# Kernel tuning notes

Measured on AMD Instinct MI355X. Metric: run time of the kernel, lower is better.

The kernel has to match this reference:

```python
import jax, jax.numpy as jnp
import numpy as np

EPS = 1e-5

def _bn(x, g, b):
    # BatchNorm1d, training-mode forward (biased batch stats)
    m = x.mean(axis=0)
    v = x.var(axis=0)
    return (x - m) * jax.lax.rsqrt(v + EPS) * g + b

def setup_inputs() -> dict:
    key = jax.random.key(0)
    ks = jax.random.split(key, 24)
    B, P, Cin, Cout, share, shrink, r = 8, 4096, 64, 128, 8, 4, 8
    k = 2 * r
    mid = Cout // shrink
    s = 0.05
    inp = {
        'points': jax.random.normal(ks[0], (B, P, 2), jnp.float32),
        'features': jax.random.normal(ks[1], (B * P, Cin), jnp.float32),
        # modules_1: Linear(2+Cin -> k), Bilinear(k,k -> k)
        'W1': jax.random.normal(ks[2], (k, 2 + Cin)) * s,
        'b1': jax.random.normal(ks[3], (k,)) * s,
        'Wb': jax.random.normal(ks[4], (k, k, k)) * s,
        'bb': jax.random.normal(ks[5], (k,)) * s,
        # linear_p: Linear(2->2, no bias), BN(2), ReLU, Linear(2->Cout)
        'Wp1': jax.random.normal(ks[6], (2, 2)) * s,
        'gp': jnp.ones((2,)), 'bp': jnp.zeros((2,)),
        'Wp2': jax.random.normal(ks[7], (Cout, 2)) * s,
        'bp2': jax.random.normal(ks[8], (Cout,)) * s,
        # modules_2: Linear(2k->mid,nb)+BN, Linear(mid->mid/share,nb)+BN, Linear(->Cout/share)
        'W2a': jax.random.normal(ks[9], (mid, 2 * k)) * s,
        'g2a': jnp.ones((mid,)), 'b2a': jnp.zeros((mid,)),
        'W2b': jax.random.normal(ks[10], (mid // share, mid)) * s,
        'g2b': jnp.ones((mid // share,)), 'b2b': jnp.zeros((mid // share,)),
        'W2c': jax.random.normal(ks[11], (Cout // share, mid // share)) * s,
        'b2c': jax.random.normal(ks[12], (Cout // share,)) * s,
        # modules_3: Linear(Cin -> Cout)
        'W3': jax.random.normal(ks[13], (Cout, Cin)) * s,
        'b3': jax.random.normal(ks[14], (Cout,)) * s,
        'radius': r,
        'share_planes': share,
    }
    return inp

def reference(points, features, W1, b1, Wb, bb, Wp1, gp, bp, Wp2, bp2,
              W2a, g2a, b2a, W2b, g2b, b2b, W2c, b2c, W3, b3,
              radius, share_planes):
    B, P, _ = points.shape
    k = 2 * radius
    # circular grouping index: neighbors (i+o) mod P, o in [-r..-1, 1..r]
    offsets = jnp.concatenate([jnp.arange(-radius, 0), jnp.arange(1, radius + 1)])
    nn = (jnp.arange(P)[:, None] + offsets[None, :]) % P            # [P, k]
    idx = (jnp.arange(B)[:, None, None] * P + nn[None]).reshape(-1) # [B*P*k]

    pts = points.reshape(-1, 2)                                     # [N, 2]
    nn_pts = pts[idx].reshape(-1, k, 2)                             # [N, k, 2]
    trans = (nn_pts - pts[:, None, :]).reshape(-1, 2)               # [N*k, 2]
    nn_feat = features[idx]                                         # [N*k, Cin]

    # modules_1: Linear -> ReLU -> Bilinear(e, e)
    e = jax.nn.relu(jnp.concatenate([trans, nn_feat], axis=1) @ W1.T + b1)
    energy = jnp.einsum('ni,oij,nj->no', e, Wb, e) + bb             # [N*k, k]

    # linear_p
    p = jax.nn.relu(_bn(trans @ Wp1.T, gp, bp))
    p_embed = p @ Wp2.T + bp2                                       # [N*k, Cout]
    Cout = p_embed.shape[1]

    # shrink_p: split Cout into (a, k), sum over a
    pe = p_embed.reshape(-1, k, Cout // k, k)
    shrink = pe.sum(axis=2).reshape(-1, k)                          # [N*k, k]

    # modules_2: MLP + softmax over neighbor axis
    w = jnp.concatenate([energy, shrink], axis=1)
    w = jax.nn.relu(_bn(w @ W2a.T, g2a, b2a))
    w = jax.nn.relu(_bn(w @ W2b.T, g2b, b2b))
    w = w @ W2c.T + b2c                                             # [N*k, Cout/share]
    w = jax.nn.softmax(w.reshape(-1, k, Cout // share_planes), axis=1)

    # modules_3 + gather + combine
    v = (features @ W3.T + b3)[idx].reshape(-1, k, Cout)
    a = v + p_embed.reshape(-1, k, Cout)
    a = a.reshape(-1, k, share_planes, Cout // share_planes)
    outputs = (a * w[:, :, None, :]).reshape(-1, k, Cout)           # [N, k, Cout]
    return outputs, trans, idx

if __name__ == '__main__':
    out = reference(**setup_inputs())
    print(out[0].shape, out[1].shape, out[2].shape)
```

## Files before the change

### kernel.cpp

```cpp
#include <hip/hip_runtime.h>

#define DEV static __device__ __forceinline__

namespace {
constexpr int PB   = 4096;
constexpr int NPTS = 32768;
constexpr int RR   = 8;
constexpr int K    = 16;
constexpr int COUT = 128;
constexpr int NK   = NPTS * K;
constexpr float BN_EPS = 1e-5f;

constexpr int    WS_SUM1 = 0;
constexpr int    WS_SUM2 = 4;
constexpr int    WS_SUM3 = 68;
constexpr size_t WS_P2   = 256;
constexpr size_t WS_W1   = WS_P2 + 2048 * 64;
constexpr size_t WS_W2   = WS_W1 + (size_t)NK * 16;
}

typedef __attribute__((ext_vector_type(8))) __bf16 bf16x8;
typedef __attribute__((ext_vector_type(4))) float  f32x4;

DEV int nbr_idx(int n, int j) {
    int b = n >> 12, i = n & (PB - 1);
    int o = (j < RR) ? (j - RR) : (j - RR + 1);
    return (b << 12) | ((i + o + PB) & (PB - 1));
}
DEV float wave_sum(float v) {
    #pragma unroll
    for (int off = 32; off >= 1; off >>= 1) v += __shfl_xor(v, off);
    return v;
}
DEV bf16x8 cvt8(float4 a, float4 b) {
    bf16x8 r;
    r[0] = (__bf16)a.x; r[1] = (__bf16)a.y; r[2] = (__bf16)a.z; r[3] = (__bf16)a.w;
    r[4] = (__bf16)b.x; r[5] = (__bf16)b.y; r[6] = (__bf16)b.z; r[7] = (__bf16)b.w;
    return r;
}
DEV float bflo(unsigned u) { union { unsigned x; float f; } c; c.x = u << 16; return c.f; }
DEV float bfhi(unsigned u) { union { unsigned x; float f; } c; c.x = u & 0xffff0000u; return c.f; }
DEV void wave_fence() {
    asm volatile("s_waitcnt lgkmcnt(0)" ::: "memory");
    __builtin_amdgcn_sched_barrier(0);
}

__global__ __launch_bounds__(256) void k_pre(const float* __restrict__ pts,
                                             const float* __restrict__ Wp1,
                                             float* __restrict__ ws)
{
    __shared__ float red[4][4];
    const int t = threadIdx.x, w = t >> 6;
    const float wp10 = Wp1[0], wp11 = Wp1[1], wp12 = Wp1[2], wp13 = Wp1[3];
    float a[4] = {0.f, 0.f, 0.f, 0.f};
    #pragma unroll
    for (int it = 0; it < 4; ++it) {
        const int row = blockIdx.x * 1024 + it * 256 + t;
        const int n = row >> 4, j = row & 15;
        const int idxr = nbr_idx(n, j);
        const float2 pn = ((const float2*)pts)[n];
        const float2 pq = ((const float2*)pts)[idxr];
        const float tx = pq.x - pn.x, ty = pq.y - pn.y;
        const float p10 = wp10 * tx + wp11 * ty;
        const float p11 = wp12 * tx + wp13 * ty;
        a[0] += p10; a[1] += p11; a[2] += p10 * p10; a[3] += p11 * p11;
    }
    #pragma unroll
    for (int q = 0; q < 4; ++q) {
        float s = wave_sum(a[q]);
        if ((t & 63) == 0) red[w][q] = s;
    }
    __syncthreads();
    if (t < 4) atomicAdd(&ws[WS_SUM1 + t], red[0][t] + red[1][t] + red[2][t] + red[3][t]);
}

__global__ __launch_bounds__(256) void k_stage1(
    const float* __restrict__ pts, const float* __restrict__ feat,
    const float* __restrict__ W1, const float* __restrict__ b1,
    const float* __restrict__ Wb, const float* __restrict__ bb,
    const float* __restrict__ Wp1, const float* __restrict__ Wp2,
    const float* __restrict__ bp2, const float* __restrict__ gp,
    const float* __restrict__ bp, const float* __restrict__ W2a,
    float* __restrict__ out_trans, float* __restrict__ out_idx,
    float* __restrict__ ws)
{
    __shared__ float es[4][16][36];
    __shared__ float sA0[16], sA1[16], sA2[16];
    __shared__ float red[4][64];

    const int t = threadIdx.x, w = t >> 6, l = t & 63, c0 = l & 15, jg = l >> 4;
    const int bid = blockIdx.x;
    const int n0 = ((bid & 7) * 256 + (bid >> 3)) * 16 + w * 4;

    if (t < 16) {
        float a0 = 0.f, a1 = 0.f, a2 = 0.f;
        for (int a8 = 0; a8 < 8; ++a8) {
            const int cc = a8 * 16 + t;
            a0 += Wp2[2 * cc]; a1 += Wp2[2 * cc + 1]; a2 += bp2[cc];
        }
        sA0[t] = a0; sA1[t] = a1; sA2[t] = a2;
    }

    const float invM = 1.f / (float)NK;
    const float m0 = ws[WS_SUM1 + 0] * invM, m1 = ws[WS_SUM1 + 1] * invM;
    const float q0 = ws[WS_SUM1 + 2] * invM, q1 = ws[WS_SUM1 + 3] * invM;
    const float sc1x = gp[0] * rsqrtf(q0 - m0 * m0 + BN_EPS);
    const float sc1y = gp[1] * rsqrtf(q1 - m1 * m1 + BN_EPS);
    const float sh1x = fmaf(-m0, sc1x, bp[0]), sh1y = fmaf(-m1, sc1y, bp[1]);
    const float wp10 = Wp1[0], wp11 = Wp1[1], wp12 = Wp1[2], wp13 = Wp1[3];

    const float w1cx = W1[c0 * 66], w1cy = W1[c0 * 66 + 1];
    const float b1c = b1[c0], bbc = bb[c0];
    bf16x8 w1b[2];
    #pragma unroll
    for (int kf = 0; kf < 2; ++kf) {
        const float* p = W1 + c0 * 66 + 2 + kf * 32 + jg * 8;
        const float2 v0 = *(const float2*)(p),     v1 = *(const float2*)(p + 2);
        const float2 v2 = *(const float2*)(p + 4), v3 = *(const float2*)(p + 6);
        w1b[kf] = cvt8(make_float4(v0.x, v0.y, v1.x, v1.y),
                       make_float4(v2.x, v2.y, v3.x, v3.y));
    }
    bf16x8 wbb[8];
    #pragma unroll
    for (int g = 0; g < 8; ++g) {
        const float4* p = (const float4*)(Wb + c0 * 256 + g * 32 + jg * 8);
        wbb[g] = cvt8(p[0], p[1]);
    }
    bf16x8 w2ab[2];
    #pragma unroll
    for (int tq = 0; tq < 2; ++tq) {
        const float4* p = (const float4*)(W2a + (c0 + 16 * tq) * 32 + jg * 8);
        w2ab[tq] = cvt8(p[0], p[1]);
    }

    int idxr[4]; float txv[4], tyv[4], ph0v[4], ph1v[4];
    bf16x8 fa0[4], fa1[4];
    #pragma unroll
    for (int nn = 0; nn < 4; ++nn) {
        const int n = n0 + nn;
        idxr[nn] = nbr_idx(n, c0);
        const float2 pn = ((const float2*)pts)[n];
        const float2 pq = ((const float2*)pts)[idxr[nn]];
        txv[nn] = pq.x - pn.x; tyv[nn] = pq.y - pn.y;
        const float p10 = wp10 * txv[nn] + wp11 * tyv[nn];
        const float p11 = wp12 * txv[nn] + wp13 * tyv[nn];
        ph0v[nn] = fmaxf(fmaf(p10, sc1x, sh1x), 0.f);
        ph1v[nn] = fmaxf(fmaf(p11, sc1y, sh1y), 0.f);
        const float4* fb = (const float4*)(feat + (size_t)idxr[nn] * 64 + jg * 8);
        fa0[nn] = cvt8(fb[0], fb[1]);
        fa1[nn] = cvt8(fb[8], fb[9]);
        if (jg == 0) {
            ((float2*)out_trans)[n * 16 + c0] = make_float2(txv[nn], tyv[nn]);
            out_idx[n * 16 + c0] = (float)idxr[nn];
        }
    }

    float s10 = 0.f, s11 = 0.f, s20 = 0.f, s21 = 0.f;
    __syncthreads();

    #pragma unroll
    for (int nn = 0; nn < 4; ++nn) {
        f32x4 acc;
        #pragma unroll
        for (int r = 0; r < 4; ++r) {
            const int row = jg * 4 + r;
            const float trx = __shfl(txv[nn], row);
            const float tryv = __shfl(tyv[nn], row);
            acc[r] = b1c + w1cx * trx + w1cy * tryv;
        }
        acc = __builtin_amdgcn_mfma_f32_16x16x32_bf16(fa0[nn], w1b[0], acc, 0, 0, 0);
        acc = __builtin_amdgcn_mfma_f32_16x16x32_bf16(fa1[nn], w1b[1], acc, 0, 0, 0);
        #pragma unroll
        for (int r = 0; r < 4; ++r) es[w][jg * 4 + r][c0] = fmaxf(acc[r], 0.f);
        wave_fence();

        const float4 ef0 = *(const float4*)&es[w][c0][0];
        const float4 ef1 = *(const float4*)&es[w][c0][4];
        const float4 ef2 = *(const float4*)&es[w][c0][8];
        const float4 ef3 = *(const float4*)&es[w][c0][12];
        const float ev[16] = {ef0.x, ef0.y, ef0.z, ef0.w, ef1.x, ef1.y, ef1.z, ef1.w,
                              ef2.x, ef2.y, ef2.z, ef2.w, ef3.x, ef3.y, ef3.z, ef3.w};
        const bool hi = (jg & 1);
        const bool ih = (jg >> 1);
        float eh[8];
        #pragma unroll
        for (int e = 0; e < 8; ++e) eh[e] = hi ? ev[8 + e] : ev[e];
        f32x4 acc2;
        #pragma unroll
        for (int r = 0; r < 4; ++r) acc2[r] = bbc;
        #pragma unroll
        for (int g = 0; g < 8; ++g) {
            const float ei = ih ? ev[2 * g + 1] : ev[2 * g];
            bf16x8 a2;
            #pragma unroll
            for (int e = 0; e < 8; ++e) a2[e] = (__bf16)(ei * eh[e]);
            acc2 = __builtin_amdgcn_mfma_f32_16x16x32_bf16(a2, wbb[g], acc2, 0, 0, 0);
        }
        #pragma unroll
        for (int r = 0; r < 4; ++r) es[w][jg * 4 + r][16 + c0] = acc2[r];
        wave_fence();

        bf16x8 xa;
        if (jg < 2) {
            const float* src = &es[w][c0][16 + jg * 8];
            #pragma unroll
            for (int e = 0; e < 8; ++e) xa[e] = (__bf16)src[e];
        } else {
            const int off = (jg - 2) * 8;
            #pragma unroll
            for (int e = 0; e < 8; ++e)
                xa[e] = (__bf16)fmaf(ph0v[nn], sA0[off + e],
                                     fmaf(ph1v[nn], sA1[off + e], sA2[off + e]));
        }
        const f32x4 z4 = {0.f, 0.f, 0.f, 0.f};
        f32x4 w1a0 = __builtin_amdgcn_mfma_f32_16x16x32_bf16(xa, w2ab[0], z4, 0, 0, 0);
        f32x4 w1a1 = __builtin_amdgcn_mfma_f32_16x16x32_bf16(xa, w2ab[1], z4, 0, 0, 0);
        #pragma unroll
        for (int r = 0; r < 4; ++r) {
            s10 += w1a0[r]; s20 += w1a0[r] * w1a0[r];
            s11 += w1a1[r]; s21 += w1a1[r] * w1a1[r];
        }
        wave_fence();

        #pragma unroll
        for (int r = 0; r < 4; ++r) {
            es[w][jg * 4 + r][c0]      = w1a0[r];
            es[w][jg * 4 + r][16 + c0] = w1a1[r];
        }
        wave_fence();

        {
            const int row = l >> 2, ch = l & 3;
            const float* src = &es[w][row][ch * 8];
            bf16x8 pk;
            #pragma unroll
            for (int e = 0; e < 8; ++e) pk[e] = (__bf16)src[e];
            reinterpret_cast<bf16x8*>(ws + WS_W1)[(size_t)((n0 + nn) * 16 + row) * 4 + ch] = pk;
        }
        wave_fence();
    }

    #pragma unroll
    for (int off = 16; off <= 32; off <<= 1) {
        s10 += __shfl_xor(s10, off); s11 += __shfl_xor(s11, off);
        s20 += __shfl_xor(s20, off); s21 += __shfl_xor(s21, off);
    }
    if (jg == 0) {
        red[w][c0] = s10; red[w][16 + c0] = s11;
        red[w][32 + c0] = s20; red[w][48 + c0] = s21;
    }
    __syncthreads();
    if (t < 64)
        (ws + WS_P2)[(size_t)bid * 64 + t] = red[0][t] + red[1][t] + red[2][t] + red[3][t];
}

__global__ __launch_bounds__(256) void k_red2(float* __restrict__ ws)
{
    __shared__ float red[4][64];
    const int t = threadIdx.x, c = t & 63, g = t >> 6;
    const float* P = ws + WS_P2;
    float s = 0.f;
    for (int r = blockIdx.x * 256 + g; r < (blockIdx.x + 1) * 256; r += 4)
        s += P[(size_t)r * 64 + c];
    red[g][c] = s;
    __syncthreads();
    if (t < 64) atomicAdd(&ws[WS_SUM2 + t], red[0][t] + red[1][t] + red[2][t] + red[3][t]);
}

__global__ __launch_bounds__(256) void k_stage3(
    const float* __restrict__ g2a, const float* __restrict__ b2a,
    const float* __restrict__ W2b, float* __restrict__ ws)
{
    __shared__ float sc2s[32], sh2s[32], w2bs[128];
    __shared__ float red[4][8];
    const int t = threadIdx.x, w = t >> 6, l = t & 63;
    if (t < 32) {
        const float invM = 1.f / (float)NK;
        const float m = ws[WS_SUM2 + t] * invM, q = ws[WS_SUM2 + 32 + t] * invM;
        const float sc = g2a[t] * rsqrtf(q - m * m + BN_EPS);
        sc2s[t] = sc; sh2s[t] = fmaf(-m, sc, b2a[t]);
    }
    if (t < 128) w2bs[t] = W2b[t];
    __syncthreads();

    const size_t row = (size_t)blockIdx.x * 256 + t;
    const uint4* w1u = reinterpret_cast<const uint4*>(ws + WS_W1) + row * 4;
    float h[32];
    #pragma unroll
    for (int i = 0; i < 4; ++i) {
        const uint4 u = w1u[i];
        h[i*8+0] = bflo(u.x); h[i*8+1] = bfhi(u.x);
        h[i*8+2] = bflo(u.y); h[i*8+3] = bfhi(u.y);
        h[i*8+4] = bflo(u.z); h[i*8+5] = bfhi(u.z);
        h[i*8+6] = bflo(u.w); h[i*8+7] = bfhi(u.w);
    }
    float acc[4] = {0.f, 0.f, 0.f, 0.f};
    #pragma unroll
    for (int q = 0; q < 32; ++q) {
        const float hv = fmaxf(fmaf(h[q], sc2s[q], sh2s[q]), 0.f);
        #pragma unroll
        for (int p = 0; p < 4; ++p) acc[p] = fmaf(w2bs[p * 32 + q], hv, acc[p]);
    }
    ((float4*)(ws + WS_W2))[row] = make_float4(acc[0], acc[1], acc[2], acc[3]);

    float r8[8] = {acc[0], acc[1], acc[2], acc[3],
                   acc[0]*acc[0], acc[1]*acc[1], acc[2]*acc[2], acc[3]*acc[3]};
    #pragma unroll
    for (int i = 0; i < 8; ++i) r8[i] = wave_sum(r8[i]);
    if (l == 0) {
        #pragma unroll
        for (int i = 0; i < 8; ++i) red[w][i] = r8[i];
    }
    __syncthreads();
    if (t < 8) atomicAdd(&ws[WS_SUM3 + t], red[0][t] + red[1][t] + red[2][t] + red[3][t]);
}

__global__ __launch_bounds__(256) void k_stage4(
    const float* __restrict__ feat, const float* __restrict__ Wp1,
    const float* __restrict__ Wp2, const float* __restrict__ bp2,
    const float* __restrict__ W2c, const float* __restrict__ b2c,
    const float* __restrict__ W3, const float* __restrict__ b3,
    const float* __restrict__ gp, const float* __restrict__ bp,
    const float* __restrict__ g2b, const float* __restrict__ b2b,
    const float* __restrict__ out_trans, const float* __restrict__ ws,
    float* __restrict__ out)
{
    __shared__ bf16x8 w3lds[1024];
    __shared__ float4 pA[32], pB[32], pC[32];
    __shared__ float4 w2c4[16];
    __shared__ float  b2cs[16];

    const int t = threadIdx.x, w = t >> 6, l = t & 63, c0 = l & 15, jg = l >> 4;
    const int bid = blockIdx.x;
    const int n0 = ((bid & 7) * 256 + (bid >> 3)) * 16 + w * 4;

    for (int f = t; f < 1024; f += 256) {
        const int s = f >> 7, kf = (f >> 6) & 1, l2 = f & 63;
        const float4* p = (const float4*)(W3 + (size_t)(16 * s + (l2 & 15)) * 64
                                          + kf * 32 + (l2 >> 4) * 8);
        w3lds[f] = cvt8(p[0], p[1]);
    }
    if (t < 32) {
        const int s = t >> 2, cc = 16 * s + (t & 3) * 4;
        pA[t] = make_float4(Wp2[2*cc], Wp2[2*cc+2], Wp2[2*cc+4], Wp2[2*cc+6]);
        pB[t] = make_float4(Wp2[2*cc+1], Wp2[2*cc+3], Wp2[2*cc+5], Wp2[2*cc+7]);
        pC[t] = make_float4(bp2[cc] + b3[cc], bp2[cc+1] + b3[cc+1],
                            bp2[cc+2] + b3[cc+2], bp2[cc+3] + b3[cc+3]);
    }
    if (t < 16) {
        w2c4[t] = make_float4(W2c[4*t], W2c[4*t+1], W2c[4*t+2], W2c[4*t+3]);
        b2cs[t] = b2c[t];
    }

    const float invM = 1.f / (float)NK;
    const float m0 = ws[WS_SUM1 + 0] * invM, m1 = ws[WS_SUM1 + 1] * invM;
    const float q0 = ws[WS_SUM1 + 2] * invM, q1 = ws[WS_SUM1 + 3] * invM;
    const float sc1x = gp[0] * rsqrtf(q0 - m0 * m0 + BN_EPS);
    const float sc1y = gp[1] * rsqrtf(q1 - m1 * m1 + BN_EPS);
    const float sh1x = fmaf(-m0, sc1x, bp[0]), sh1y = fmaf(-m1, sc1y, bp[1]);
    const float wp10 = Wp1[0], wp11 = Wp1[1], wp12 = Wp1[2], wp13 = Wp1[3];
    float sc3[4], sh3[4];
    #pragma unroll
    for (int p = 0; p < 4; ++p) {
        const float m = ws[WS_SUM3 + p] * invM, q = ws[WS_SUM3 + 4 + p] * invM;
        sc3[p] = g2b[p] * rsqrtf(q - m * m + BN_EPS);
        sh3[p] = fmaf(-m, sc3[p], b2b[p]);
    }

    int idxr[4]; float2 trv[4]; float4 qv[4];
    bf16x8 fa0[4], fa1[4];
    #pragma unroll
    for (int nn = 0; nn < 4; ++nn) {
        const int n = n0 + nn;
        idxr[nn] = nbr_idx(n, c0);
        const float4* fb = (const float4*)(feat + (size_t)idxr[nn] * 64 + jg * 8);
        fa0[nn] = cvt8(fb[0], fb[1]);
        fa1[nn] = cvt8(fb[8], fb[9]);
        trv[nn] = ((const float2*)out_trans)[n * 16 + c0];
        qv[nn]  = ((const float4*)(ws + WS_W2))[n * 16 + c0];
    }
    __syncthreads();

    #pragma unroll
    for (int nn = 0; nn < 4; ++nn) {
        const int n = n0 + nn;
        const float p10 = wp10 * trv[nn].x + wp11 * trv[nn].y;
        const float p11 = wp12 * trv[nn].x + wp13 * trv[nn].y;
        const float ph0 = fmaxf(fmaf(p10, sc1x, sh1x), 0.f);
        const float ph1 = fmaxf(fmaf(p11, sc1y, sh1y), 0.f);
        const float h0 = fmaxf(fmaf(qv[nn].x, sc3[0], sh3[0]), 0.f);
        const float h1 = fmaxf(fmaf(qv[nn].y, sc3[1], sh3[1]), 0.f);
        const float h2 = fmaxf(fmaf(qv[nn].z, sc3[2], sh3[2]), 0.f);
        const float h3 = fmaxf(fmaf(qv[nn].w, sc3[3], sh3[3]), 0.f);
        float wsm[4];
        #pragma unroll
        for (int r = 0; r < 4; ++r) {
            const int c = jg * 4 + r;
            const float4 wc = w2c4[c];
            const float lgv = b2cs[c] + wc.x * h0 + wc.y * h1 + wc.z * h2 + wc.w * h3;
            float mx = lgv;
            #pragma unroll
            for (int off = 1; off <= 8; off <<= 1) mx = fmaxf(mx, __shfl_xor(mx, off));
            const float ex = __expf(lgv - mx);
            float ss = ex;
            #pragma unroll
            for (int off = 1; off <= 8; off <<= 1) ss += __shfl_xor(ss, off);
            wsm[r] = ex / ss;
        }
        float* ob = out + (size_t)(n * 16 + c0) * COUT;
        #pragma unroll
        for (int s = 0; s < 8; ++s) {
            const float4 a4 = pA[s * 4 + jg], b4 = pB[s * 4 + jg], c4 = pC[s * 4 + jg];
            f32x4 ci;
            ci[0] = fmaf(ph0, a4.x, fmaf(ph1, b4.x, c4.x));
            ci[1] = fmaf(ph0, a4.y, fmaf(ph1, b4.y, c4.y));
            ci[2] = fmaf(ph0, a4.z, fmaf(ph1, b4.z, c4.z));
            ci[3] = fmaf(ph0, a4.w, fmaf(ph1, b4.w, c4.w));
            ci = __builtin_amdgcn_mfma_f32_16x16x32_bf16(w3lds[s * 128 + l],      fa0[nn], ci, 0, 0, 0);
            ci = __builtin_amdgcn_mfma_f32_16x16x32_bf16(w3lds[s * 128 + 64 + l], fa1[nn], ci, 0, 0, 0);
            *(float4*)(ob + 16 * s + jg * 4) =
                make_float4(ci[0] * wsm[0], ci[1] * wsm[1], ci[2] * wsm[2], ci[3] * wsm[3]);
        }
    }
}

extern "C" void kernel_launch(void* const* d_in, const int* in_sizes, int n_in,
                              void* d_out, int out_size, void* d_ws, size_t ws_size,
                              hipStream_t stream)
{
    const float* pts  = (const float*)d_in[0];
    const float* feat = (const float*)d_in[1];
    const float* W1   = (const float*)d_in[2];
    const float* b1   = (const float*)d_in[3];
    const float* Wb   = (const float*)d_in[4];
    const float* bb   = (const float*)d_in[5];
    const float* Wp1  = (const float*)d_in[6];
    const float* gp   = (const float*)d_in[7];
    const float* bp   = (const float*)d_in[8];
    const float* Wp2  = (const float*)d_in[9];
    const float* bp2  = (const float*)d_in[10];
    const float* W2a  = (const float*)d_in[11];
    const float* g2a  = (const float*)d_in[12];
    const float* b2a  = (const float*)d_in[13];
    const float* W2b  = (const float*)d_in[14];
    const float* g2b  = (const float*)d_in[15];
    const float* b2b  = (const float*)d_in[16];
    const float* W2c  = (const float*)d_in[17];
    const float* b2c  = (const float*)d_in[18];
    const float* W3   = (const float*)d_in[19];
    const float* b3   = (const float*)d_in[20];

    float* out       = (float*)d_out;
    float* out_trans = out + (size_t)NK * COUT;
    float* out_idx   = out_trans + (size_t)NK * 2;
    float* ws        = (float*)d_ws;

    hipMemsetAsync(ws, 0, 256 * sizeof(float), stream);
    k_pre<<<512, 256, 0, stream>>>(pts, Wp1, ws);
    k_stage1<<<2048, 256, 0, stream>>>(pts, feat, W1, b1, Wb, bb, Wp1, Wp2, bp2,
                                       gp, bp, W2a, out_trans, out_idx, ws);
    k_red2<<<8, 256, 0, stream>>>(ws);
    k_stage3<<<2048, 256, 0, stream>>>(g2a, b2a, W2b, ws);
    k_stage4<<<2048, 256, 0, stream>>>(feat, Wp1, Wp2, bp2, W2c, b2c, W3, b3,
                                       gp, bp, g2b, b2b, out_trans, ws, out);
}
```

Measured before the change: 260.2 us.

## Fuse all stages into one persistent kernel with software grid barriers

Replaces the five separate launches (pre-stats, stage1, partial reduction, stage3, stage4) with one persistent kernel of 512 blocks. The blocks synchronise through atomic-counter grid barriers in the workspace, and BN statistics are accumulated with direct atomics instead of a separate reduction kernel. The final stage double-buffers neighbour loads, and the softmax max-subtraction is dropped. This removes launch gaps and tail effects. The cost is reliance on all 512 blocks being co-resident, and on the barrier counter being reset by the memset, otherwise the barriers could deadlock. Removing the max-subtraction also risks exp overflow.

```diff
diff --git a/kernel.cpp b/kernel.cpp
--- a/kernel.cpp
+++ b/kernel.cpp
@@ -9,13 +9,15 @@
 constexpr int K    = 16;
 constexpr int COUT = 128;
 constexpr int NK   = NPTS * K;
+constexpr int GRID = 512;
+constexpr int NPB  = NPTS / GRID;
 constexpr float BN_EPS = 1e-5f;
 
 constexpr int    WS_SUM1 = 0;
 constexpr int    WS_SUM2 = 4;
 constexpr int    WS_SUM3 = 68;
-constexpr size_t WS_P2   = 256;
-constexpr size_t WS_W1   = WS_P2 + 2048 * 64;
+constexpr int    WS_BAR  = 96;
+constexpr size_t WS_W1   = 256;
 constexpr size_t WS_W2   = WS_W1 + (size_t)NK * 16;
 }
 
@@ -45,52 +47,54 @@
     __builtin_amdgcn_sched_barrier(0);
 }
 
-__global__ __launch_bounds__(256) void k_pre(const float* __restrict__ pts,
-                                             const float* __restrict__ Wp1,
-                                             float* __restrict__ ws)
-{
-    __shared__ float red[4][4];
-    const int t = threadIdx.x, w = t >> 6;
-    const float wp10 = Wp1[0], wp11 = Wp1[1], wp12 = Wp1[2], wp13 = Wp1[3];
-    float a[4] = {0.f, 0.f, 0.f, 0.f};
-    #pragma unroll
-    for (int it = 0; it < 4; ++it) {
-        const int row = blockIdx.x * 1024 + it * 256 + t;
-        const int n = row >> 4, j = row & 15;
-        const int idxr = nbr_idx(n, j);
-        const float2 pn = ((const float2*)pts)[n];
-        const float2 pq = ((const float2*)pts)[idxr];
-        const float tx = pq.x - pn.x, ty = pq.y - pn.y;
-        const float p10 = wp10 * tx + wp11 * ty;
-        const float p11 = wp12 * tx + wp13 * ty;
-        a[0] += p10; a[1] += p11; a[2] += p10 * p10; a[3] += p11 * p11;
-    }
-    #pragma unroll
-    for (int q = 0; q < 4; ++q) {
-        float s = wave_sum(a[q]);
-        if ((t & 63) == 0) red[w][q] = s;
-    }
+DEV void grid_barrier(int* cnt) {
     __syncthreads();
-    if (t < 4) atomicAdd(&ws[WS_SUM1 + t], red[0][t] + red[1][t] + red[2][t] + red[3][t]);
-}
-
-__global__ __launch_bounds__(256) void k_stage1(
+    if (threadIdx.x == 0) {
+        __threadfence();
+        __hip_atomic_fetch_add(cnt, 1, __ATOMIC_ACQ_REL, __HIP_MEMORY_SCOPE_AGENT);
+        int spins = 0;
+        while (__hip_atomic_load(cnt, __ATOMIC_ACQUIRE, __HIP_MEMORY_SCOPE_AGENT) < GRID
+               && spins < (1 << 24)) {
+            __builtin_amdgcn_s_sleep(2);
+            ++spins;
+        }
+        __threadfence();
+    }
+    __syncthreads();
+}
+
+__global__ __launch_bounds__(256, 2) void k_mega(
     const float* __restrict__ pts, const float* __restrict__ feat,
     const float* __restrict__ W1, const float* __restrict__ b1,
     const float* __restrict__ Wb, const float* __restrict__ bb,
-    const float* __restrict__ Wp1, const float* __restrict__ Wp2,
-    const float* __restrict__ bp2, const float* __restrict__ gp,
-    const float* __restrict__ bp, const float* __restrict__ W2a,
-    float* __restrict__ out_trans, float* __restrict__ out_idx,
-    float* __restrict__ ws)
+    const float* __restrict__ Wp1, const float* __restrict__ gp,
+    const float* __restrict__ bp, const float* __restrict__ Wp2,
+    const float* __restrict__ bp2, const float* __restrict__ W2a,
+    const float* __restrict__ g2a, const float* __restrict__ b2a,
+    const float* __restrict__ W2b, const float* __restrict__ g2b,
+    const float* __restrict__ b2b, const float* __restrict__ W2c,
+    const float* __restrict__ b2c, const float* __restrict__ W3,
+    const float* __restrict__ b3,
+    float* __restrict__ out, float* __restrict__ out_trans,
+    float* __restrict__ out_idx, float* __restrict__ ws)
 {
-    __shared__ float es[4][16][36];
-    __shared__ float sA0[16], sA1[16], sA2[16];
-    __shared__ float red[4][64];
+    __shared__ float  es[4][16][36];
+    __shared__ float  sA0[16], sA1[16], sA2[16];
+    __shared__ float  redl[4][64];
+    __shared__ bf16x8 w3lds[1024];
+    __shared__ float4 pA[32], pB[32], pC[32];
+    __shared__ float4 w2c4[16];
+    __shared__ float  b2cs[16];
+    __shared__ float  sc2s[32], sh2s[32], w2bs[128];
 
     const int t = threadIdx.x, w = t >> 6, l = t & 63, c0 = l & 15, jg = l >> 4;
     const int bid = blockIdx.x;
-    const int n0 = ((bid & 7) * 256 + (bid >> 3)) * 16 + w * 4;
+    const int swz = (bid & 7) * (GRID / 8) + (bid >> 3);
+    const int n_base = swz * NPB;
+    int* bar = (int*)(ws + WS_BAR);
+
+    const float wp10 = Wp1[0], wp11 = Wp1[1], wp12 = Wp1[2], wp13 = Wp1[3];
+    const float invM = 1.f / (float)NK;
 
     if (t < 16) {
         float a0 = 0.f, a1 = 0.f, a2 = 0.f;
@@ -101,326 +105,314 @@
         sA0[t] = a0; sA1[t] = a1; sA2[t] = a2;
     }
 
-    const float invM = 1.f / (float)NK;
-    const float m0 = ws[WS_SUM1 + 0] * invM, m1 = ws[WS_SUM1 + 1] * invM;
-    const float q0 = ws[WS_SUM1 + 2] * invM, q1 = ws[WS_SUM1 + 3] * invM;
-    const float sc1x = gp[0] * rsqrtf(q0 - m0 * m0 + BN_EPS);
-    const float sc1y = gp[1] * rsqrtf(q1 - m1 * m1 + BN_EPS);
-    const float sh1x = fmaf(-m0, sc1x, bp[0]), sh1y = fmaf(-m1, sc1y, bp[1]);
-    const float wp10 = Wp1[0], wp11 = Wp1[1], wp12 = Wp1[2], wp13 = Wp1[3];
-
-    const float w1cx = W1[c0 * 66], w1cy = W1[c0 * 66 + 1];
-    const float b1c = b1[c0], bbc = bb[c0];
-    bf16x8 w1b[2];
-    #pragma unroll
-    for (int kf = 0; kf < 2; ++kf) {
-        const float* p = W1 + c0 * 66 + 2 + kf * 32 + jg * 8;
-        const float2 v0 = *(const float2*)(p),     v1 = *(const float2*)(p + 2);
-        const float2 v2 = *(const float2*)(p + 4), v3 = *(const float2*)(p + 6);
-        w1b[kf] = cvt8(make_float4(v0.x, v0.y, v1.x, v1.y),
-                       make_float4(v2.x, v2.y, v3.x, v3.y));
-    }
-    bf16x8 wbb[8];
-    #pragma unroll
-    for (int g = 0; g < 8; ++g) {
-        const float4* p = (const float4*)(Wb + c0 * 256 + g * 32 + jg * 8);
-        wbb[g] = cvt8(p[0], p[1]);
-    }
-    bf16x8 w2ab[2];
-    #pragma unroll
-    for (int tq = 0; tq < 2; ++tq) {
-        const float4* p = (const float4*)(W2a + (c0 + 16 * tq) * 32 + jg * 8);
-        w2ab[tq] = cvt8(p[0], p[1]);
-    }
-
-    int idxr[4]; float txv[4], tyv[4], ph0v[4], ph1v[4];
-    bf16x8 fa0[4], fa1[4];
-    #pragma unroll
-    for (int nn = 0; nn < 4; ++nn) {
-        const int n = n0 + nn;
-        idxr[nn] = nbr_idx(n, c0);
-        const float2 pn = ((const float2*)pts)[n];
-        const float2 pq = ((const float2*)pts)[idxr[nn]];
-        txv[nn] = pq.x - pn.x; tyv[nn] = pq.y - pn.y;
-        const float p10 = wp10 * txv[nn] + wp11 * tyv[nn];
-        const float p11 = wp12 * txv[nn] + wp13 * tyv[nn];
-        ph0v[nn] = fmaxf(fmaf(p10, sc1x, sh1x), 0.f);
-        ph1v[nn] = fmaxf(fmaf(p11, sc1y, sh1y), 0.f);
-        const float4* fb = (const float4*)(feat + (size_t)idxr[nn] * 64 + jg * 8);
-        fa0[nn] = cvt8(fb[0], fb[1]);
-        fa1[nn] = cvt8(fb[8], fb[9]);
-        if (jg == 0) {
-            ((float2*)out_trans)[n * 16 + c0] = make_float2(txv[nn], tyv[nn]);
-            out_idx[n * 16 + c0] = (float)idxr[nn];
-        }
-    }
-
-    float s10 = 0.f, s11 = 0.f, s20 = 0.f, s21 = 0.f;
-    __syncthreads();
-
-    #pragma unroll
-    for (int nn = 0; nn < 4; ++nn) {
-        f32x4 acc;
-        #pragma unroll
-        for (int r = 0; r < 4; ++r) {
-            const int row = jg * 4 + r;
-            const float trx = __shfl(txv[nn], row);
-            const float tryv = __shfl(tyv[nn], row);
-            acc[r] = b1c + w1cx * trx + w1cy * tryv;
-        }
-        acc = __builtin_amdgcn_mfma_f32_16x16x32_bf16(fa0[nn], w1b[0], acc, 0, 0, 0);
-        acc = __builtin_amdgcn_mfma_f32_16x16x32_bf16(fa1[nn], w1b[1], acc, 0, 0, 0);
-        #pragma unroll
-        for (int r = 0; r < 4; ++r) es[w][jg * 4 + r][c0] = fmaxf(acc[r], 0.f);
-        wave_fence();
-
-        const float4 ef0 = *(const float4*)&es[w][c0][0];
-        const float4 ef1 = *(const float4*)&es[w][c0][4];
-        const float4 ef2 = *(const float4*)&es[w][c0][8];
-        const float4 ef3 = *(const float4*)&es[w][c0][12];
-        const float ev[16] = {ef0.x, ef0.y, ef0.z, ef0.w, ef1.x, ef1.y, ef1.z, ef1.w,
-                              ef2.x, ef2.y, ef2.z, ef2.w, ef3.x, ef3.y, ef3.z, ef3.w};
+    {
+        float a[4] = {0.f, 0.f, 0.f, 0.f};
+        #pragma unroll
+        for (int it = 0; it < 4; ++it) {
+            const int row = n_base * 16 + it * 256 + t;
+            const int n = row >> 4, j = row & 15;
+            const int idxr = nbr_idx(n, j);
+            const float2 pn = ((const float2*)pts)[n];
+            const float2 pq = ((const float2*)pts)[idxr];
+            const float tx = pq.x - pn.x, ty = pq.y - pn.y;
+            const float p10 = wp10 * tx + wp11 * ty;
+            const float p11 = wp12 * tx + wp13 * ty;
+            a[0] += p10; a[1] += p11; a[2] += p10 * p10; a[3] += p11 * p11;
+        }
+        #pragma unroll
+        for (int q = 0; q < 4; ++q) {
+            float s = wave_sum(a[q]);
+            if (l == 0) redl[w][q] = s;
+        }
+        __syncthreads();
+        if (t < 4) atomicAdd(&ws[WS_SUM1 + t],
+                             redl[0][t] + redl[1][t] + redl[2][t] + redl[3][t]);
+    }
+    grid_barrier(bar + 0);
+
+    {
+        const float w1cx = W1[c0 * 66], w1cy = W1[c0 * 66 + 1];
+        const float b1c = b1[c0], bbc = bb[c0];
+        bf16x8 w1b[2];
+        #pragma unroll
+        for (int kf = 0; kf < 2; ++kf) {
+            const float* p = W1 + c0 * 66 + 2 + kf * 32 + jg * 8;
+            const float2 v0 = *(const float2*)(p),     v1 = *(const float2*)(p + 2);
+            const float2 v2 = *(const float2*)(p + 4), v3 = *(const float2*)(p + 6);
+            w1b[kf] = cvt8(make_float4(v0.x, v0.y, v1.x, v1.y),
+                           make_float4(v2.x, v2.y, v3.x, v3.y));
+        }
+        bf16x8 wbb[8];
+        #pragma unroll
+        for (int g = 0; g < 8; ++g) {
+            const float4* p = (const float4*)(Wb + c0 * 256 + g * 32 + jg * 8);
+            wbb[g] = cvt8(p[0], p[1]);
+        }
+        bf16x8 w2ab[2];
+        #pragma unroll
+        for (int tq = 0; tq < 2; ++tq) {
+            const float4* p = (const float4*)(W2a + (c0 + 16 * tq) * 32 + jg * 8);
+            w2ab[tq] = cvt8(p[0], p[1]);
+        }
+
+        const float m0 = ws[WS_SUM1 + 0] * invM, m1 = ws[WS_SUM1 + 1] * invM;
+        const float q0 = ws[WS_SUM1 + 2] * invM, q1 = ws[WS_SUM1 + 3] * invM;
+        const float sc1x = gp[0] * rsqrtf(q0 - m0 * m0 + BN_EPS);
+        const float sc1y = gp[1] * rsqrtf(q1 - m1 * m1 + BN_EPS);
+        const float sh1x = fmaf(-m0, sc1x, bp[0]), sh1y = fmaf(-m1, sc1y, bp[1]);
+
+        float s10 = 0.f, s11 = 0.f, s20 = 0.f, s21 = 0.f;
         const bool hi = (jg & 1);
         const bool ih = (jg >> 1);
-        float eh[8];
-        #pragma unroll
-        for (int e = 0; e < 8; ++e) eh[e] = hi ? ev[8 + e] : ev[e];
-        f32x4 acc2;
-        #pragma unroll
-        for (int r = 0; r < 4; ++r) acc2[r] = bbc;
-        #pragma unroll
-        for (int g = 0; g < 8; ++g) {
-            const float ei = ih ? ev[2 * g + 1] : ev[2 * g];
-            bf16x8 a2;
-            #pragma unroll
-            for (int e = 0; e < 8; ++e) a2[e] = (__bf16)(ei * eh[e]);
-            acc2 = __builtin_amdgcn_mfma_f32_16x16x32_bf16(a2, wbb[g], acc2, 0, 0, 0);
-        }
-        #pragma unroll
-        for (int r = 0; r < 4; ++r) es[w][jg * 4 + r][16 + c0] = acc2[r];
-        wave_fence();
-
-        bf16x8 xa;
-        if (jg < 2) {
-            const float* src = &es[w][c0][16 + jg * 8];
-            #pragma unroll
-            for (int e = 0; e < 8; ++e) xa[e] = (__bf16)src[e];
-        } else {
-            const int off = (jg - 2) * 8;
-            #pragma unroll
-            for (int e = 0; e < 8; ++e)
-                xa[e] = (__bf16)fmaf(ph0v[nn], sA0[off + e],
-                                     fmaf(ph1v[nn], sA1[off + e], sA2[off + e]));
-        }
-        const f32x4 z4 = {0.f, 0.f, 0.f, 0.f};
-        f32x4 w1a0 = __builtin_amdgcn_mfma_f32_16x16x32_bf16(xa, w2ab[0], z4, 0, 0, 0);
-        f32x4 w1a1 = __builtin_amdgcn_mfma_f32_16x16x32_bf16(xa, w2ab[1], z4, 0, 0, 0);
-        #pragma unroll
-        for (int r = 0; r < 4; ++r) {
-            s10 += w1a0[r]; s20 += w1a0[r] * w1a0[r];
-            s11 += w1a1[r]; s21 += w1a1[r] * w1a1[r];
-        }
-        wave_fence();
-
-        #pragma unroll
-        for (int r = 0; r < 4; ++r) {
-            es[w][jg * 4 + r][c0]      = w1a0[r];
-            es[w][jg * 4 + r][16 + c0] = w1a1[r];
-        }
-        wave_fence();
-
-        {
-            const int row = l >> 2, ch = l & 3;
-            const float* src = &es[w][row][ch * 8];
-            bf16x8 pk;
-            #pragma unroll
-            for (int e = 0; e < 8; ++e) pk[e] = (__bf16)src[e];
-            reinterpret_cast<bf16x8*>(ws + WS_W1)[(size_t)((n0 + nn) * 16 + row) * 4 + ch] = pk;
-        }
-        wave_fence();
-    }
-
-    #pragma unroll
-    for (int off = 16; off <= 32; off <<= 1) {
-        s10 += __shfl_xor(s10, off); s11 += __shfl_xor(s11, off);
-        s20 += __shfl_xor(s20, off); s21 += __shfl_xor(s21, off);
-    }
-    if (jg == 0) {
-        red[w][c0] = s10; red[w][16 + c0] = s11;
-        red[w][32 + c0] = s20; red[w][48 + c0] = s21;
-    }
-    __syncthreads();
-    if (t < 64)
-        (ws + WS_P2)[(size_t)bid * 64 + t] = red[0][t] + red[1][t] + red[2][t] + red[3][t];
-}
-
-__global__ __launch_bounds__(256) void k_red2(float* __restrict__ ws)
-{
-    __shared__ float red[4][64];
-    const int t = threadIdx.x, c = t & 63, g = t >> 6;
-    const float* P = ws + WS_P2;
-    float s = 0.f;
-    for (int r = blockIdx.x * 256 + g; r < (blockIdx.x + 1) * 256; r += 4)
-        s += P[(size_t)r * 64 + c];
-    red[g][c] = s;
-    __syncthreads();
-    if (t < 64) atomicAdd(&ws[WS_SUM2 + t], red[0][t] + red[1][t] + red[2][t] + red[3][t]);
-}
-
-__global__ __launch_bounds__(256) void k_stage3(
-    const float* __restrict__ g2a, const float* __restrict__ b2a,
-    const float* __restrict__ W2b, float* __restrict__ ws)
-{
-    __shared__ float sc2s[32], sh2s[32], w2bs[128];
-    __shared__ float red[4][8];
-    const int t = threadIdx.x, w = t >> 6, l = t & 63;
-    if (t < 32) {
-        const float invM = 1.f / (float)NK;
-        const float m = ws[WS_SUM2 + t] * invM, q = ws[WS_SUM2 + 32 + t] * invM;
-        const float sc = g2a[t] * rsqrtf(q - m * m + BN_EPS);
-        sc2s[t] = sc; sh2s[t] = fmaf(-m, sc, b2a[t]);
-    }
-    if (t < 128) w2bs[t] = W2b[t];
-    __syncthreads();
-
-    const size_t row = (size_t)blockIdx.x * 256 + t;
-    const uint4* w1u = reinterpret_cast<const uint4*>(ws + WS_W1) + row * 4;
-    float h[32];
-    #pragma unroll
-    for (int i = 0; i < 4; ++i) {
-        const uint4 u = w1u[i];
-        h[i*8+0] = bflo(u.x); h[i*8+1] = bfhi(u.x);
-        h[i*8+2] = bflo(u.y); h[i*8+3] = bfhi(u.y);
-        h[i*8+4] = bflo(u.z); h[i*8+5] = bfhi(u.z);
-        h[i*8+6] = bflo(u.w); h[i*8+7] = bfhi(u.w);
-    }
-    float acc[4] = {0.f, 0.f, 0.f, 0.f};
-    #pragma unroll
-    for (int q = 0; q < 32; ++q) {
-        const float hv = fmaxf(fmaf(h[q], sc2s[q], sh2s[q]), 0.f);
-        #pragma unroll
-        for (int p = 0; p < 4; ++p) acc[p] = fmaf(w2bs[p * 32 + q], hv, acc[p]);
-    }
-    ((float4*)(ws + WS_W2))[row] = make_float4(acc[0], acc[1], acc[2], acc[3]);
-
-    float r8[8] = {acc[0], acc[1], acc[2], acc[3],
-                   acc[0]*acc[0], acc[1]*acc[1], acc[2]*acc[2], acc[3]*acc[3]};
-    #pragma unroll
-    for (int i = 0; i < 8; ++i) r8[i] = wave_sum(r8[i]);
-    if (l == 0) {
-        #pragma unroll
-        for (int i = 0; i < 8; ++i) red[w][i] = r8[i];
-    }
-    __syncthreads();
-    if (t < 8) atomicAdd(&ws[WS_SUM3 + t], red[0][t] + red[1][t] + red[2][t] + red[3][t]);
-}
-
-__global__ __launch_bounds__(256) void k_stage4(
-    const float* __restrict__ feat, const float* __restrict__ Wp1,
-    const float* __restrict__ Wp2, const float* __restrict__ bp2,
-    const float* __restrict__ W2c, const float* __restrict__ b2c,
-    const float* __restrict__ W3, const float* __restrict__ b3,
-    const float* __restrict__ gp, const float* __restrict__ bp,
-    const float* __restrict__ g2b, const float* __restrict__ b2b,
-    const float* __restrict__ out_trans, const float* __restrict__ ws,
-    float* __restrict__ out)
-{
-    __shared__ bf16x8 w3lds[1024];
-    __shared__ float4 pA[32], pB[32], pC[32];
-    __shared__ float4 w2c4[16];
-    __shared__ float  b2cs[16];
-
-    const int t = threadIdx.x, w = t >> 6, l = t & 63, c0 = l & 15, jg = l >> 4;
-    const int bid = blockIdx.x;
-    const int n0 = ((bid & 7) * 256 + (bid >> 3)) * 16 + w * 4;
-
-    for (int f = t; f < 1024; f += 256) {
-        const int s = f >> 7, kf = (f >> 6) & 1, l2 = f & 63;
-        const float4* p = (const float4*)(W3 + (size_t)(16 * s + (l2 & 15)) * 64
-                                          + kf * 32 + (l2 >> 4) * 8);
-        w3lds[f] = cvt8(p[0], p[1]);
-    }
-    if (t < 32) {
-        const int s = t >> 2, cc = 16 * s + (t & 3) * 4;
-        pA[t] = make_float4(Wp2[2*cc], Wp2[2*cc+2], Wp2[2*cc+4], Wp2[2*cc+6]);
-        pB[t] = make_float4(Wp2[2*cc+1], Wp2[2*cc+3], Wp2[2*cc+5], Wp2[2*cc+7]);
-        pC[t] = make_float4(bp2[cc] + b3[cc], bp2[cc+1] + b3[cc+1],
-                            bp2[cc+2] + b3[cc+2], bp2[cc+3] + b3[cc+3]);
-    }
-    if (t < 16) {
-        w2c4[t] = make_float4(W2c[4*t], W2c[4*t+1], W2c[4*t+2], W2c[4*t+3]);
-        b2cs[t] = b2c[t];
-    }
-
-    const float invM = 1.f / (float)NK;
-    const float m0 = ws[WS_SUM1 + 0] * invM, m1 = ws[WS_SUM1 + 1] * invM;
-    const float q0 = ws[WS_SUM1 + 2] * invM, q1 = ws[WS_SUM1 + 3] * invM;
-    const float sc1x = gp[0] * rsqrtf(q0 - m0 * m0 + BN_EPS);
-    const float sc1y = gp[1] * rsqrtf(q1 - m1 * m1 + BN_EPS);
-    const float sh1x = fmaf(-m0, sc1x, bp[0]), sh1y = fmaf(-m1, sc1y, bp[1]);
-    const float wp10 = Wp1[0], wp11 = Wp1[1], wp12 = Wp1[2], wp13 = Wp1[3];
-    float sc3[4], sh3[4];
-    #pragma unroll
-    for (int p = 0; p < 4; ++p) {
-        const float m = ws[WS_SUM3 + p] * invM, q = ws[WS_SUM3 + 4 + p] * invM;
-        sc3[p] = g2b[p] * rsqrtf(q - m * m + BN_EPS);
-        sh3[p] = fmaf(-m, sc3[p], b2b[p]);
-    }
-
-    int idxr[4]; float2 trv[4]; float4 qv[4];
-    bf16x8 fa0[4], fa1[4];
-    #pragma unroll
-    for (int nn = 0; nn < 4; ++nn) {
-        const int n = n0 + nn;
-        idxr[nn] = nbr_idx(n, c0);
-        const float4* fb = (const float4*)(feat + (size_t)idxr[nn] * 64 + jg * 8);
-        fa0[nn] = cvt8(fb[0], fb[1]);
-        fa1[nn] = cvt8(fb[8], fb[9]);
-        trv[nn] = ((const float2*)out_trans)[n * 16 + c0];
-        qv[nn]  = ((const float4*)(ws + WS_W2))[n * 16 + c0];
-    }
-    __syncthreads();
-
-    #pragma unroll
-    for (int nn = 0; nn < 4; ++nn) {
-        const int n = n0 + nn;
-        const float p10 = wp10 * trv[nn].x + wp11 * trv[nn].y;
-        const float p11 = wp12 * trv[nn].x + wp13 * trv[nn].y;
-        const float ph0 = fmaxf(fmaf(p10, sc1x, sh1x), 0.f);
-        const float ph1 = fmaxf(fmaf(p11, sc1y, sh1y), 0.f);
-        const float h0 = fmaxf(fmaf(qv[nn].x, sc3[0], sh3[0]), 0.f);
-        const float h1 = fmaxf(fmaf(qv[nn].y, sc3[1], sh3[1]), 0.f);
-        const float h2 = fmaxf(fmaf(qv[nn].z, sc3[2], sh3[2]), 0.f);
-        const float h3 = fmaxf(fmaf(qv[nn].w, sc3[3], sh3[3]), 0.f);
-        float wsm[4];
-        #pragma unroll
-        for (int r = 0; r < 4; ++r) {
-            const int c = jg * 4 + r;
-            const float4 wc = w2c4[c];
-            const float lgv = b2cs[c] + wc.x * h0 + wc.y * h1 + wc.z * h2 + wc.w * h3;
-            float mx = lgv;
-            #pragma unroll
-            for (int off = 1; off <= 8; off <<= 1) mx = fmaxf(mx, __shfl_xor(mx, off));
-            const float ex = __expf(lgv - mx);
-            float ss = ex;
-            #pragma unroll
-            for (int off = 1; off <= 8; off <<= 1) ss += __shfl_xor(ss, off);
-            wsm[r] = ex / ss;
-        }
-        float* ob = out + (size_t)(n * 16 + c0) * COUT;
-        #pragma unroll
-        for (int s = 0; s < 8; ++s) {
-            const float4 a4 = pA[s * 4 + jg], b4 = pB[s * 4 + jg], c4 = pC[s * 4 + jg];
-            f32x4 ci;
-            ci[0] = fmaf(ph0, a4.x, fmaf(ph1, b4.x, c4.x));
-            ci[1] = fmaf(ph0, a4.y, fmaf(ph1, b4.y, c4.y));
-            ci[2] = fmaf(ph0, a4.z, fmaf(ph1, b4.z, c4.z));
-            ci[3] = fmaf(ph0, a4.w, fmaf(ph1, b4.w, c4.w));
-            ci = __builtin_amdgcn_mfma_f32_16x16x32_bf16(w3lds[s * 128 + l],      fa0[nn], ci, 0, 0, 0);
-            ci = __builtin_amdgcn_mfma_f32_16x16x32_bf16(w3lds[s * 128 + 64 + l], fa1[nn], ci, 0, 0, 0);
-            *(float4*)(ob + 16 * s + jg * 4) =
-                make_float4(ci[0] * wsm[0], ci[1] * wsm[1], ci[2] * wsm[2], ci[3] * wsm[3]);
-        }
+
+        for (int i = 0; i < 16; ++i) {
+            const int n = n_base + w * 16 + i;
+            const int idxr = nbr_idx(n, c0);
+            const float2 pn = ((const float2*)pts)[n];
+            const float2 pq = ((const float2*)pts)[idxr];
+            const float tx = pq.x - pn.x, ty = pq.y - pn.y;
+            if (jg == 0) {
+                ((float2*)out_trans)[n * 16 + c0] = make_float2(tx, ty);
+                out_idx[n * 16 + c0] = (float)idxr;
+            }
+            const float p10 = wp10 * tx + wp11 * ty;
+            const float p11 = wp12 * tx + wp13 * ty;
+            const float ph0 = fmaxf(fmaf(p10, sc1x, sh1x), 0.f);
+            const float ph1 = fmaxf(fmaf(p11, sc1y, sh1y), 0.f);
+            const float4* fb = (const float4*)(feat + (size_t)idxr * 64 + jg * 8);
+            const bf16x8 fa0 = cvt8(fb[0], fb[1]);
+            const bf16x8 fa1 = cvt8(fb[8], fb[9]);
+
+            f32x4 acc;
+            #pragma unroll
+            for (int r = 0; r < 4; ++r) {
+                const int row = jg * 4 + r;
+                const float trx  = __shfl(tx, row);
+                const float tryv = __shfl(ty, row);
+                acc[r] = b1c + w1cx * trx + w1cy * tryv;
+            }
+            acc = __builtin_amdgcn_mfma_f32_16x16x32_bf16(fa0, w1b[0], acc, 0, 0, 0);
+            acc = __builtin_amdgcn_mfma_f32_16x16x32_bf16(fa1, w1b[1], acc, 0, 0, 0);
+            #pragma unroll
+            for (int r = 0; r < 4; ++r) es[w][jg * 4 + r][c0] = fmaxf(acc[r], 0.f);
+            wave_fence();
+
+            const float4 ef0 = *(const float4*)&es[w][c0][0];
+            const float4 ef1 = *(const float4*)&es[w][c0][4];
+            const float4 ef2 = *(const float4*)&es[w][c0][8];
+            const float4 ef3 = *(const float4*)&es[w][c0][12];
+            const float ev[16] = {ef0.x, ef0.y, ef0.z, ef0.w, ef1.x, ef1.y, ef1.z, ef1.w,
+                                  ef2.x, ef2.y, ef2.z, ef2.w, ef3.x, ef3.y, ef3.z, ef3.w};
+            float eh[8];
+            #pragma unroll
+            for (int e = 0; e < 8; ++e) eh[e] = hi ? ev[8 + e] : ev[e];
+            f32x4 acc2;
+            #pragma unroll
+            for (int r = 0; r < 4; ++r) acc2[r] = bbc;
+            #pragma unroll
+            for (int g = 0; g < 8; ++g) {
+                const float ei = ih ? ev[2 * g + 1] : ev[2 * g];
+                bf16x8 a2;
+                #pragma unroll
+                for (int e = 0; e < 8; ++e) a2[e] = (__bf16)(ei * eh[e]);
+                acc2 = __builtin_amdgcn_mfma_f32_16x16x32_bf16(a2, wbb[g], acc2, 0, 0, 0);
+            }
+            #pragma unroll
+            for (int r = 0; r < 4; ++r) es[w][jg * 4 + r][16 + c0] = acc2[r];
+            wave_fence();
+
+            bf16x8 xa;
+            if (jg < 2) {
+                const float* src = &es[w][c0][16 + jg * 8];
+                #pragma unroll
+                for (int e = 0; e < 8; ++e) xa[e] = (__bf16)src[e];
+            } else {
+                const int off = (jg - 2) * 8;
+                #pragma unroll
+                for (int e = 0; e < 8; ++e)
+                    xa[e] = (__bf16)fmaf(ph0, sA0[off + e],
+                                         fmaf(ph1, sA1[off + e], sA2[off + e]));
+            }
+            const f32x4 z4 = {0.f, 0.f, 0.f, 0.f};
+            f32x4 w1a0 = __builtin_amdgcn_mfma_f32_16x16x32_bf16(xa, w2ab[0], z4, 0, 0, 0);
+            f32x4 w1a1 = __builtin_amdgcn_mfma_f32_16x16x32_bf16(xa, w2ab[1], z4, 0, 0, 0);
+            #pragma unroll
+            for (int r = 0; r < 4; ++r) {
+                s10 += w1a0[r]; s20 += w1a0[r] * w1a0[r];
+                s11 += w1a1[r]; s21 += w1a1[r] * w1a1[r];
+            }
+            wave_fence();
+
+            #pragma unroll
+            for (int r = 0; r < 4; ++r) {
+                es[w][jg * 4 + r][c0]      = w1a0[r];
+                es[w][jg * 4 + r][16 + c0] = w1a1[r];
+            }
+            wave_fence();
+
+            {
+                const int row = l >> 2, ch = l & 3;
+                const float* src = &es[w][row][ch * 8];
+                bf16x8 pk;
+                #pragma unroll
+                for (int e = 0; e < 8; ++e) pk[e] = (__bf16)src[e];
+                reinterpret_cast<bf16x8*>(ws + WS_W1)[(size_t)(n * 16 + row) * 4 + ch] = pk;
+            }
+            wave_fence();
+        }
+
+        #pragma unroll
+        for (int off = 16; off <= 32; off <<= 1) {
+            s10 += __shfl_xor(s10, off); s11 += __shfl_xor(s11, off);
+            s20 += __shfl_xor(s20, off); s21 += __shfl_xor(s21, off);
+        }
+        __syncthreads();
+        if (jg == 0) {
+            redl[w][c0] = s10; redl[w][16 + c0] = s11;
+            redl[w][32 + c0] = s20; redl[w][48 + c0] = s21;
+        }
+        __syncthreads();
+        if (t < 64) atomicAdd(&ws[WS_SUM2 + t],
+                              redl[0][t] + redl[1][t] + redl[2][t] + redl[3][t]);
+    }
+    grid_barrier(bar + 1);
+
+    {
+        if (t < 32) {
+            const float m = ws[WS_SUM2 + t] * invM, q = ws[WS_SUM2 + 32 + t] * invM;
+            const float sc = g2a[t] * rsqrtf(q - m * m + BN_EPS);
+            sc2s[t] = sc; sh2s[t] = fmaf(-m, sc, b2a[t]);
+        }
+        if (t < 128) w2bs[t] = W2b[t];
+        __syncthreads();
+
+        float r8[8] = {0.f, 0.f, 0.f, 0.f, 0.f, 0.f, 0.f, 0.f};
+        #pragma unroll
+        for (int it = 0; it < 4; ++it) {
+            const size_t row = (size_t)n_base * 16 + it * 256 + t;
+            const uint4* w1u = reinterpret_cast<const uint4*>(ws + WS_W1) + row * 4;
+            float h[32];
+            #pragma unroll
+            for (int i = 0; i < 4; ++i) {
+                const uint4 u = w1u[i];
+                h[i*8+0] = bflo(u.x); h[i*8+1] = bfhi(u.x);
+                h[i*8+2] = bflo(u.y); h[i*8+3] = bfhi(u.y);
+                h[i*8+4] = bflo(u.z); h[i*8+5] = bfhi(u.z);
+                h[i*8+6] = bflo(u.w); h[i*8+7] = bfhi(u.w);
+            }
+            float acc[4] = {0.f, 0.f, 0.f, 0.f};
+            #pragma unroll
+            for (int q = 0; q < 32; ++q) {
+                const float hv = fmaxf(fmaf(h[q], sc2s[q], sh2s[q]), 0.f);
+                #pragma unroll
+                for (int p = 0; p < 4; ++p) acc[p] = fmaf(w2bs[p * 32 + q], hv, acc[p]);
+            }
+            ((float4*)(ws + WS_W2))[row] = make_float4(acc[0], acc[1], acc[2], acc[3]);
+            #pragma unroll
+            for (int p = 0; p < 4; ++p) { r8[p] += acc[p]; r8[4 + p] += acc[p] * acc[p]; }
+        }
+        #pragma unroll
+        for (int i = 0; i < 8; ++i) r8[i] = wave_sum(r8[i]);
+        __syncthreads();
+        if (l == 0) {
+            #pragma unroll
+            for (int i = 0; i < 8; ++i) redl[w][i] = r8[i];
+        }
+        __syncthreads();
+        if (t < 8) atomicAdd(&ws[WS_SUM3 + t],
+                             redl[0][t] + redl[1][t] + redl[2][t] + redl[3][t]);
+    }
+    grid_barrier(bar + 2);
+
+    {
+        for (int f = t; f < 1024; f += 256) {
+            const int s = f >> 7, kf = (f >> 6) & 1, l2 = f & 63;
+            const float4* p = (const float4*)(W3 + (size_t)(16 * s + (l2 & 15)) * 64
+                                              + kf * 32 + (l2 >> 4) * 8);
+            w3lds[f] = cvt8(p[0], p[1]);
+        }
+        if (t < 32) {
+            const int s = t >> 2, cc = 16 * s + (t & 3) * 4;
+            pA[t] = make_float4(Wp2[2*cc], Wp2[2*cc+2], Wp2[2*cc+4], Wp2[2*cc+6]);
+            pB[t] = make_float4(Wp2[2*cc+1], Wp2[2*cc+3], Wp2[2*cc+5], Wp2[2*cc+7]);
+            pC[t] = make_float4(bp2[cc] + b3[cc], bp2[cc+1] + b3[cc+1],
+                                bp2[cc+2] + b3[cc+2], bp2[cc+3] + b3[cc+3]);
+        }
+        if (t < 16) {
+            w2c4[t] = make_float4(W2c[4*t], W2c[4*t+1], W2c[4*t+2], W2c[4*t+3]);
+            b2cs[t] = b2c[t];
+        }
+
+        const float m0 = ws[WS_SUM1 + 0] * invM, m1 = ws[WS_SUM1 + 1] * invM;
+        const float q0 = ws[WS_SUM1 + 2] * invM, q1 = ws[WS_SUM1 + 3] * invM;
+        const float sc1x = gp[0] * rsqrtf(q0 - m0 * m0 + BN_EPS);
+        const float sc1y = gp[1] * rsqrtf(q1 - m1 * m1 + BN_EPS);
+        const float sh1x = fmaf(-m0, sc1x, bp[0]), sh1y = fmaf(-m1, sc1y, bp[1]);
+        float sc3[4], sh3[4];
+        #pragma unroll
+        for (int p = 0; p < 4; ++p) {
+            const float m = ws[WS_SUM3 + p] * invM, q = ws[WS_SUM3 + 4 + p] * invM;
+            sc3[p] = g2b[p] * rsqrtf(q - m * m + BN_EPS);
+            sh3[p] = fmaf(-m, sc3[p], b2b[p]);
+        }
+        __syncthreads();
+
+        const int nw0 = n_base + w * 16;
+        int idxr2[2]; float2 trv2[2]; float4 qv2[2];
+        bf16x8 f02[2], f12[2];
+
+        #define LOADC(i, b) { \
+            const int n_ = nw0 + (i); \
+            idxr2[b] = nbr_idx(n_, c0); \
+            const float4* fb_ = (const float4*)(feat + (size_t)idxr2[b] * 64 + jg * 8); \
+            f02[b] = cvt8(fb_[0], fb_[1]); \
+            f12[b] = cvt8(fb_[8], fb_[9]); \
+            trv2[b] = ((const float2*)out_trans)[n_ * 16 + c0]; \
+            qv2[b] = ((const float4*)(ws + WS_W2))[n_ * 16 + c0]; }
+
+        LOADC(0, 0)
+        #pragma unroll
+        for (int i = 0; i < 16; ++i) {
+            const int b = i & 1;
+            if (i < 15) LOADC(i + 1, b ^ 1)
+            const int n = nw0 + i;
+
+            const float p10 = wp10 * trv2[b].x + wp11 * trv2[b].y;
+            const float p11 = wp12 * trv2[b].x + wp13 * trv2[b].y;
+            const float ph0 = fmaxf(fmaf(p10, sc1x, sh1x), 0.f);
+            const float ph1 = fmaxf(fmaf(p11, sc1y, sh1y), 0.f);
+            const float h0 = fmaxf(fmaf(qv2[b].x, sc3[0], sh3[0]), 0.f);
+            const float h1 = fmaxf(fmaf(qv2[b].y, sc3[1], sh3[1]), 0.f);
+            const float h2 = fmaxf(fmaf(qv2[b].z, sc3[2], sh3[2]), 0.f);
+            const float h3 = fmaxf(fmaf(qv2[b].w, sc3[3], sh3[3]), 0.f);
+            float wsm[4];
+            #pragma unroll
+            for (int r = 0; r < 4; ++r) {
+                const int c = jg * 4 + r;
+                const float4 wc = w2c4[c];
+                const float lgv = b2cs[c] + wc.x * h0 + wc.y * h1 + wc.z * h2 + wc.w * h3;
+                const float ex = __expf(lgv);
+                float ss = ex;
+                #pragma unroll
+                for (int off = 1; off <= 8; off <<= 1) ss += __shfl_xor(ss, off);
+                wsm[r] = ex / ss;
+            }
+            float* ob = out + (size_t)(n * 16 + c0) * COUT;
+            #pragma unroll
+            for (int s = 0; s < 8; ++s) {
+                const float4 a4 = pA[s * 4 + jg], b4 = pB[s * 4 + jg], c4 = pC[s * 4 + jg];
+                f32x4 ci;
+                ci[0] = fmaf(ph0, a4.x, fmaf(ph1, b4.x, c4.x));
+                ci[1] = fmaf(ph0, a4.y, fmaf(ph1, b4.y, c4.y));
+                ci[2] = fmaf(ph0, a4.z, fmaf(ph1, b4.z, c4.z));
+                ci[3] = fmaf(ph0, a4.w, fmaf(ph1, b4.w, c4.w));
+                ci = __builtin_amdgcn_mfma_f32_16x16x32_bf16(w3lds[s * 128 + l],      f02[b], ci, 0, 0, 0);
+                ci = __builtin_amdgcn_mfma_f32_16x16x32_bf16(w3lds[s * 128 + 64 + l], f12[b], ci, 0, 0, 0);
+                *(float4*)(ob + 16 * s + jg * 4) =
+                    make_float4(ci[0] * wsm[0], ci[1] * wsm[1], ci[2] * wsm[2], ci[3] * wsm[3]);
+            }
+        }
+        #undef LOADC
     }
 }
 
@@ -456,11 +448,7 @@
     float* ws        = (float*)d_ws;
 
     hipMemsetAsync(ws, 0, 256 * sizeof(float), stream);
-    k_pre<<<512, 256, 0, stream>>>(pts, Wp1, ws);
-    k_stage1<<<2048, 256, 0, stream>>>(pts, feat, W1, b1, Wb, bb, Wp1, Wp2, bp2,
-                                       gp, bp, W2a, out_trans, out_idx, ws);
-    k_red2<<<8, 256, 0, stream>>>(ws);
-    k_stage3<<<2048, 256, 0, stream>>>(g2a, b2a, W2b, ws);
-    k_stage4<<<2048, 256, 0, stream>>>(feat, Wp1, Wp2, bp2, W2c, b2c, W3, b3,
-                                       gp, bp, g2b, b2b, out_trans, ws, out);
-}
+    k_mega<<<GRID, 256, 0, stream>>>(pts, feat, W1, b1, Wb, bb, Wp1, gp, bp,
+                                     Wp2, bp2, W2a, g2a, b2a, W2b, g2b, b2b,
+                                     W2c, b2c, W3, b3, out, out_trans, out_idx, ws);
+}
```

New measurement: 333.5 us. 28.2% more time.
